# Optimization experiments

Hardware: AMD Instinct MI355X
Metric: run time of the kernel (lower is better)

## Reference

```python
import jax, jax.numpy as jnp
import numpy as np
from jax.scipy.special import logsumexp

D, E, V = 512, 4, 32000
B, L = 1, 1024


def setup_inputs() -> dict:
    key = jax.random.key(0)
    ks = jax.random.split(key, 5)
    s = 0.02
    return {
        "hidden_states": jax.random.normal(ks[0], (B, L, D), dtype=jnp.float32),
        "W_prior": jax.random.normal(ks[1], (D, E), dtype=jnp.float32) * s,
        "b_prior": jnp.zeros((E,), dtype=jnp.float32),
        "W_latent": jax.random.normal(ks[2], (D, E * D), dtype=jnp.float32) * s,
        "b_latent": jnp.zeros((E * D,), dtype=jnp.float32),
        "W_dec": jax.random.normal(ks[3], (D, V), dtype=jnp.float32) * s,
        "b_dec": jnp.zeros((V,), dtype=jnp.float32),
    }


def reference(hidden_states, W_prior, b_prior, W_latent, b_latent, W_dec, b_dec):
    # hidden_states: [B, L, D]
    b, l, d = hidden_states.shape
    e = W_prior.shape[1]
    # mixture coefficients (split_hidden=False path): softmax over experts
    mix_logits = hidden_states @ W_prior + b_prior                 # [B, L, E]
    log_coef = jax.nn.log_softmax(mix_logits, axis=-1)             # [B, L, E]
    # per-expert latent projections with tanh
    latent = jnp.tanh(hidden_states @ W_latent + b_latent)         # [B, L, E*D]
    latent = latent.reshape(b, l, e, d)                            # [B, L, E, D]
    # shared decoder to vocab
    logits = jnp.einsum("bled,dv->blev", latent, W_dec) + b_dec    # [B, L, E, V]
    logp = jax.nn.log_softmax(logits, axis=-1)                     # [B, L, E, V]
    # log(sum_e coef_e * softmax_e) == logsumexp_e(log_coef_e + log_softmax_e)
    out = logsumexp(logp + log_coef[..., None], axis=2)            # [B, L, V]
    return out
```

## Files before the change

kernel.cpp:

```cpp
#include <hip/hip_runtime.h>
#include <hip/hip_bf16.h>
#include <hip/hip_fp16.h>
#include <math.h>


#define D_ 512
#define E_ 4
#define V_ 32000
#define L_ 1024
#define AROWS (L_ * E_)

#define SA_ 0x7D7D7D7D
#define SB_ 0x7B7B7B7B

typedef __attribute__((ext_vector_type(8))) short s16x8;
typedef __attribute__((ext_vector_type(4))) float f32x4;
typedef __attribute__((ext_vector_type(2))) float f32x2;
typedef __attribute__((ext_vector_type(4))) int i32x4;
typedef __attribute__((ext_vector_type(8))) int i32x8;
typedef __attribute__((ext_vector_type(4))) unsigned int u32x4;
typedef const __attribute__((address_space(1))) char* gp1_t;
typedef __attribute__((address_space(3))) char* lp3_t;

__device__ __forceinline__ void gload_lds16(const void* g, void* l) {
  __builtin_amdgcn_global_load_lds((gp1_t)g, (lp3_t)l, 16, 0, 0);
}

#define PREP_DEC  8000
#define PREP_LAT  (PREP_DEC + 1024)
#define PREP_CVT  (PREP_LAT + 512)
#define PREP_PRI  (PREP_CVT + 256)
#define PREP_TOT  (PREP_PRI + 16)

__global__ __launch_bounds__(256) void prep_kernel(
    const float* __restrict__ hs, const float* __restrict__ W_prior,
    const float* __restrict__ b_prior, const float* __restrict__ W_latent,
    const float* __restrict__ W_dec,
    __hip_bfloat16* __restrict__ hs_bf, __hip_bfloat16* __restrict__ WlatT,
    unsigned char* __restrict__ WdecT8, float* __restrict__ log_coef,
    float* __restrict__ S) {
  __shared__ float tileS[64 * 33];
  const int b = blockIdx.x;
  const int tid = threadIdx.x;

  if (b < PREP_DEC) {
    const int vb = (b % 1000) * 32;
    const int db = (b / 1000) * 64;
    {
      const int r = tid >> 2, c0 = (tid & 3) * 8;
      const float* src = W_dec + (size_t)(db + r) * V_ + vb + c0;
      float4 a0 = *(const float4*)src;
      float4 a1 = *(const float4*)(src + 4);
      float* t = &tileS[r * 33 + c0];
      t[0] = a0.x; t[1] = a0.y; t[2] = a0.z; t[3] = a0.w;
      t[4] = a1.x; t[5] = a1.y; t[6] = a1.z; t[7] = a1.w;
    }
    __syncthreads();
    {
      const int vr = tid >> 3, d0 = (tid & 7) * 8;
      float t8[8];
      #pragma unroll
      for (int j = 0; j < 8; ++j) t8[j] = tileS[(d0 + j) * 33 + vr] * 16.f;
      unsigned int u0 = 0, u1 = 0;
      u0 = __builtin_amdgcn_cvt_pk_fp8_f32(t8[0], t8[1], u0, false);
      u0 = __builtin_amdgcn_cvt_pk_fp8_f32(t8[2], t8[3], u0, true);
      u1 = __builtin_amdgcn_cvt_pk_fp8_f32(t8[4], t8[5], u1, false);
      u1 = __builtin_amdgcn_cvt_pk_fp8_f32(t8[6], t8[7], u1, true);
      uint2 uu = {u0, u1};
      *(uint2*)&WdecT8[(size_t)(vb + vr) * D_ + db + d0] = uu;
    }
  } else if (b < PREP_LAT) {
    const int bb = b - PREP_DEC;
    const int cb = (bb & 63) * 32, rb = (bb >> 6) * 32;
    const int C = E_ * D_, R = D_;
    const int tx = tid & 31, ty = tid >> 5;
    #pragma unroll
    for (int j = 0; j < 32; j += 8)
      tileS[(ty + j) * 33 + tx] = W_latent[(size_t)(rb + ty + j) * C + cb + tx];
    __syncthreads();
    #pragma unroll
    for (int j = 0; j < 32; j += 8)
      WlatT[(size_t)(cb + ty + j) * R + rb + tx] = __float2bfloat16(tileS[tx * 33 + ty + j]);
  } else if (b < PREP_CVT) {
    int i = ((b - PREP_LAT) * 256 + tid) * 4;
    float4 v = *(const float4*)(hs + i);
    hs_bf[i + 0] = __float2bfloat16(v.x);
    hs_bf[i + 1] = __float2bfloat16(v.y);
    hs_bf[i + 2] = __float2bfloat16(v.z);
    hs_bf[i + 3] = __float2bfloat16(v.w);
  } else if (b < PREP_PRI) {
    int t = (b - PREP_CVT) * 4 + (tid >> 6);
    int lane = tid & 63;
    float a0 = 0.f, a1 = 0.f, a2 = 0.f, a3 = 0.f;
    for (int d = lane; d < D_; d += 64) {
      float h = hs[t * D_ + d];
      float4 w = ((const float4*)W_prior)[d];
      a0 += h * w.x; a1 += h * w.y; a2 += h * w.z; a3 += h * w.w;
    }
    #pragma unroll
    for (int off = 32; off > 0; off >>= 1) {
      a0 += __shfl_xor(a0, off);
      a1 += __shfl_xor(a1, off);
      a2 += __shfl_xor(a2, off);
      a3 += __shfl_xor(a3, off);
    }
    a0 += b_prior[0]; a1 += b_prior[1]; a2 += b_prior[2]; a3 += b_prior[3];
    float mx = fmaxf(fmaxf(a0, a1), fmaxf(a2, a3));
    float ls = mx + logf(expf(a0 - mx) + expf(a1 - mx) + expf(a2 - mx) + expf(a3 - mx));
    if (lane == 0) {
      log_coef[t * 4 + 0] = a0 - ls;
      log_coef[t * 4 + 1] = a1 - ls;
      log_coef[t * 4 + 2] = a2 - ls;
      log_coef[t * 4 + 3] = a3 - ls;
    }
  } else {
    S[(b - PREP_PRI) * 256 + tid] = 0.f;
  }
}

__global__ void qk_kernel(const float* __restrict__ log_coef, const float* __restrict__ S,
                          float* __restrict__ q) {
  int i = blockIdx.x * blockDim.x + threadIdx.x;
  if (i < AROWS) q[i] = __expf(log_coef[i]) / S[i];
}

__global__ __launch_bounds__(256, 2) void latent_gemm(
    const __hip_bfloat16* __restrict__ Abf, const __hip_bfloat16* __restrict__ BT,
    const float* __restrict__ b_latent, unsigned char* __restrict__ latent8) {
  __shared__ short As[128 * 32];
  __shared__ short Bs[128 * 32];
  const int tid = threadIdx.x;
  const int wave = tid >> 6, lane = tid & 63;
  const int wm = wave >> 1, wn = wave & 1;
  const int m0 = blockIdx.y * 128;
  const int n0 = blockIdx.x * 128;
  const int lrow = lane & 15;
  const int kgrp = lane >> 4;
  const int srow = wave * 16 + (lane >> 2);
  const int scol = (lane & 3) * 8;

  f32x4 acc[4][4];
  #pragma unroll
  for (int mt = 0; mt < 4; ++mt)
    #pragma unroll
    for (int nt = 0; nt < 4; ++nt) acc[mt][nt] = f32x4{0.f, 0.f, 0.f, 0.f};

  for (int kt = 0; kt < 16; ++kt) {
    const int k0 = kt * 32;
    #pragma unroll
    for (int j = 0; j < 2; ++j) {
      const int row = j * 64 + srow;
      gload_lds16(Abf + (size_t)(m0 + row) * D_ + k0 + scol, &As[(j * 256 + wave * 64) * 8]);
      gload_lds16(BT + (size_t)(n0 + row) * D_ + k0 + scol, &Bs[(j * 256 + wave * 64) * 8]);
    }
    __syncthreads();
    s16x8 af[4], bfr[4];
    #pragma unroll
    for (int mt = 0; mt < 4; ++mt) af[mt] = *(const s16x8*)&As[(wm * 64 + mt * 16 + lrow) * 32 + kgrp * 8];
    #pragma unroll
    for (int nt = 0; nt < 4; ++nt) bfr[nt] = *(const s16x8*)&Bs[(wn * 64 + nt * 16 + lrow) * 32 + kgrp * 8];
    #pragma unroll
    for (int mt = 0; mt < 4; ++mt)
      #pragma unroll
      for (int nt = 0; nt < 4; ++nt)
        acc[mt][nt] = __builtin_amdgcn_mfma_f32_16x16x32_bf16(af[mt], bfr[nt], acc[mt][nt], 0, 0, 0);
    __syncthreads();
  }

  float blat[4];
  #pragma unroll
  for (int nt = 0; nt < 4; ++nt) blat[nt] = b_latent[n0 + wn * 64 + nt * 16 + lrow];
  #pragma unroll
  for (int mt = 0; mt < 4; ++mt)
    #pragma unroll
    for (int r = 0; r < 4; ++r) {
      const int row = m0 + wm * 64 + mt * 16 + kgrp * 4 + r;
      #pragma unroll
      for (int nt = 0; nt < 4; ++nt) {
        const int col = n0 + wn * 64 + nt * 16 + lrow;
        float v = tanhf(acc[mt][nt][r] + blat[nt]) * 4.f;
        int u = __builtin_amdgcn_cvt_pk_fp8_f32(v, v, 0, false);
        latent8[(size_t)row * (E_ * D_) + col] = (unsigned char)(u & 0xff);
      }
    }
}

template <int MODE>
__global__ __launch_bounds__(256, 2) void mos_gemm(
    const unsigned char* __restrict__ A8,
    const unsigned char* __restrict__ W8,
    const float* __restrict__ b_dec,
    const float* __restrict__ q,
    float* __restrict__ S,
    float* __restrict__ out,
    unsigned int* __restrict__ pbuf) {
  const int bid = blockIdx.x;
  const int xcd = bid & 7;
  const int idx = bid >> 3;
  const int mg = xcd >> 2;
  const int vg = xcd & 3;
  const int vt = vg * 63 + (idx >> 4);
  const int mtile = mg * 16 + (idx & 15);
  if (vt >= V_ / 128) return;
  const int m0 = mtile * 128;
  const int v0 = vt * 128;

  __shared__ __attribute__((aligned(16))) unsigned char As[128 * 128];
  __shared__ __attribute__((aligned(16))) unsigned char Bs[128 * 128];
  const int tid = threadIdx.x;
  const int wave = tid >> 6, lane = tid & 63;
  const int wm = wave >> 1, wn = wave & 1;
  const int lrow = lane & 15;
  const int kgrp = lane >> 4;
  const int srow8 = wave * 8 + (lane >> 3);
  const int schunk = lane & 7;

  float bdec[4];
  #pragma unroll
  for (int nt = 0; nt < 4; ++nt) bdec[nt] = b_dec[v0 + wn * 64 + nt * 16 + lrow];

  f32x4 acc[4][4];
  #pragma unroll
  for (int mt = 0; mt < 4; ++mt)
    #pragma unroll
    for (int nt = 0; nt < 4; ++nt) acc[mt][nt] = f32x4{0.f, 0.f, 0.f, 0.f};

  for (int kt = 0; kt < 4; ++kt) {
    const int kb = kt * 128;
    #pragma unroll
    for (int j = 0; j < 4; ++j) {
      const int row = j * 32 + srow8;
      const int sc = (schunk ^ (row & 7)) * 16;
      gload_lds16(A8 + (size_t)(m0 + row) * D_ + kb + sc, &As[(j * 32 + wave * 8) * 128]);
      gload_lds16(W8 + (size_t)(v0 + row) * D_ + kb + sc, &Bs[(j * 32 + wave * 8) * 128]);
    }
    __syncthreads();
    i32x8 af[4], bfr[4];
    #pragma unroll
    for (int mt = 0; mt < 4; ++mt) {
      const int row = wm * 64 + mt * 16 + lrow;
      const int s = lrow & 7;
      i32x4 lo = *(const i32x4*)&As[row * 128 + (((kgrp * 2) ^ s) * 16)];
      i32x4 hi = *(const i32x4*)&As[row * 128 + (((kgrp * 2 + 1) ^ s) * 16)];
      af[mt] = __builtin_shufflevector(lo, hi, 0, 1, 2, 3, 4, 5, 6, 7);
    }
    #pragma unroll
    for (int nt = 0; nt < 4; ++nt) {
      const int row = wn * 64 + nt * 16 + lrow;
      const int s = lrow & 7;
      i32x4 lo = *(const i32x4*)&Bs[row * 128 + (((kgrp * 2) ^ s) * 16)];
      i32x4 hi = *(const i32x4*)&Bs[row * 128 + (((kgrp * 2 + 1) ^ s) * 16)];
      bfr[nt] = __builtin_shufflevector(lo, hi, 0, 1, 2, 3, 4, 5, 6, 7);
    }
    #pragma unroll
    for (int mt = 0; mt < 4; ++mt)
      #pragma unroll
      for (int nt = 0; nt < 4; ++nt)
        acc[mt][nt] = __builtin_amdgcn_mfma_scale_f32_16x16x128_f8f6f4(
            af[mt], bfr[nt], acc[mt][nt], 0, 0, 0, SA_, 0, SB_);
    __syncthreads();
  }

  if constexpr (MODE == 1 || MODE == 3) {
    #pragma unroll
    for (int mt = 0; mt < 4; ++mt) {
      const int row4 = m0 + wm * 64 + mt * 16 + kgrp * 4;
      const int token = row4 >> 2;
      float p0 = 0.f, p1 = 0.f, p2 = 0.f, p3 = 0.f;
      #pragma unroll
      for (int nt = 0; nt < 4; ++nt) {
        float e0 = __expf(acc[mt][nt][0] + bdec[nt]);
        float e1 = __expf(acc[mt][nt][1] + bdec[nt]);
        float e2 = __expf(acc[mt][nt][2] + bdec[nt]);
        float e3 = __expf(acc[mt][nt][3] + bdec[nt]);
        p0 += e0; p1 += e1; p2 += e2; p3 += e3;
        if constexpr (MODE == 3) {
          const int v = v0 + wn * 64 + nt * 16 + lrow;
          int u = 0;
          u = __builtin_amdgcn_cvt_pk_fp8_f32(e0, e1, u, false);
          u = __builtin_amdgcn_cvt_pk_fp8_f32(e2, e3, u, true);
          __builtin_nontemporal_store((unsigned int)u, &pbuf[(size_t)token * V_ + v]);
        }
      }
      #pragma unroll
      for (int off = 1; off < 16; off <<= 1) {
        p0 += __shfl_xor(p0, off);
        p1 += __shfl_xor(p1, off);
        p2 += __shfl_xor(p2, off);
        p3 += __shfl_xor(p3, off);
      }
      if (lrow == 0) {
        atomicAdd(&S[row4 + 0], p0);
        atomicAdd(&S[row4 + 1], p1);
        atomicAdd(&S[row4 + 2], p2);
        atomicAdd(&S[row4 + 3], p3);
      }
    }
  } else {
    #pragma unroll
    for (int mt = 0; mt < 4; ++mt) {
      const int row4 = m0 + wm * 64 + mt * 16 + kgrp * 4;
      const float4 qv = *(const float4*)&q[row4];
      const int token = row4 >> 2;
      #pragma unroll
      for (int nt = 0; nt < 4; ++nt) {
        float v = qv.x * __expf(acc[mt][nt][0] + bdec[nt]) +
                  qv.y * __expf(acc[mt][nt][1] + bdec[nt]) +
                  qv.z * __expf(acc[mt][nt][2] + bdec[nt]) +
                  qv.w * __expf(acc[mt][nt][3] + bdec[nt]);
        out[(size_t)token * V_ + v0 + wn * 64 + nt * 16 + lrow] = __logf(v);
      }
    }
  }
}

__global__ __launch_bounds__(256) void combine_kernel(
    const unsigned int* __restrict__ pbuf,
    const float* __restrict__ lc, const float* __restrict__ S,
    float* __restrict__ out) {
  const int t = blockIdx.y;
  const int v = blockIdx.x * 1024 + threadIdx.x * 4;
  if (v >= V_) return;
  const float4 lcv = ((const float4*)lc)[t];
  const float4 Sv = ((const float4*)S)[t];
  const float q0 = __expf(lcv.x) / Sv.x;
  const float q1 = __expf(lcv.y) / Sv.y;
  const float q2 = __expf(lcv.z) / Sv.z;
  const float q3 = __expf(lcv.w) / Sv.w;
  u32x4 u = __builtin_nontemporal_load((const u32x4*)(pbuf + (size_t)t * V_ + v));
  float4 o;
  #pragma unroll
  for (int j = 0; j < 4; ++j) {
    unsigned int w = u[j];
    f32x2 lo = __builtin_amdgcn_cvt_pk_f32_fp8(w, false);
    f32x2 hi = __builtin_amdgcn_cvt_pk_f32_fp8(w, true);
    float s = q0 * lo.x + q1 * lo.y + q2 * hi.x + q3 * hi.y;
    ((float*)&o)[j] = __logf(s);
  }
  *(float4*)&out[(size_t)t * V_ + v] = o;
}

extern "C" void kernel_launch(void* const* d_in, const int* in_sizes, int n_in,
                              void* d_out, int out_size, void* d_ws, size_t ws_size,
                              hipStream_t stream) {
  const float* hs       = (const float*)d_in[0];
  const float* W_prior  = (const float*)d_in[1];
  const float* b_prior  = (const float*)d_in[2];
  const float* W_latent = (const float*)d_in[3];
  const float* b_latent = (const float*)d_in[4];
  const float* W_dec    = (const float*)d_in[5];
  const float* b_dec    = (const float*)d_in[6];
  float* out = (float*)d_out;

  char* ws = (char*)d_ws;
  __hip_bfloat16* hs_bf   = (__hip_bfloat16*)(ws);
  __hip_bfloat16* WlatT   = (__hip_bfloat16*)(ws + (1u << 20));
  unsigned char*  latent8 = (unsigned char*)(ws + 3u * (1u << 20));
  unsigned char*  WdecT8  = (unsigned char*)(ws + 5u * (1u << 20));
  float* log_coef = (float*)(ws + 22u * (1u << 20));
  float* S = log_coef + AROWS;
  float* q = S + AROWS;
  unsigned int* pbuf = (unsigned int*)(ws + 23u * (1u << 20));

  const size_t needA = 23u * (1u << 20) + (size_t)L_ * V_ * 4;
  const bool pathA = ws_size >= needA;

  prep_kernel<<<PREP_TOT, 256, 0, stream>>>(hs, W_prior, b_prior, W_latent, W_dec,
                                            hs_bf, WlatT, WdecT8, log_coef, S);
  latent_gemm<<<dim3((E_ * D_) / 128, L_ / 128), 256, 0, stream>>>(hs_bf, WlatT, b_latent, latent8);

  if (pathA) {
    mos_gemm<3><<<8 * 16 * 63, 256, 0, stream>>>(latent8, WdecT8, b_dec, nullptr, S, nullptr, pbuf);
    combine_kernel<<<dim3(32, L_), 256, 0, stream>>>(pbuf, log_coef, S, out);
  } else {
    mos_gemm<1><<<8 * 16 * 63, 256, 0, stream>>>(latent8, WdecT8, b_dec, nullptr, S, nullptr, nullptr);
    qk_kernel<<<(AROWS + 255) / 256, 256, 0, stream>>>(log_coef, S, q);
    mos_gemm<2><<<8 * 16 * 63, 256, 0, stream>>>(latent8, WdecT8, b_dec, q, nullptr, out, nullptr);
  }
}
```

Before: 357.9 us.

## Use fragment-native LDS layout, DPP row reductions, and MFMA priority in decoder GEMM

Each lane now loads its own MFMA fragment directly from global memory into LDS, so fragments are read back with contiguous lane-indexed accesses and no XOR swizzle or per-row address math. The k-loop is fully unrolled, and s_setprio raises wave priority around the MFMA block. The 16-lane shuffle-xor reduction of the partial exp sums becomes a DPP row_shr prefix sum, with lane 15 doing the atomics. This targets LDS bank conflicts, address arithmetic and reduction overhead. The cost is uncoalesced global reads, since each lane now fetches 16 bytes from a different row.

```diff
diff --git a/kernel.cpp b/kernel.cpp
--- a/kernel.cpp
+++ b/kernel.cpp
@@ -24,6 +24,19 @@
 
 __device__ __forceinline__ void gload_lds16(const void* g, void* l) {
   __builtin_amdgcn_global_load_lds((gp1_t)g, (lp3_t)l, 16, 0, 0);
+}
+
+__device__ __forceinline__ float dpp_row16_sum(float x) {
+  int t;
+  t = __builtin_amdgcn_update_dpp(0, __float_as_int(x), 0x111, 0xF, 0xF, true);
+  x += __int_as_float(t);
+  t = __builtin_amdgcn_update_dpp(0, __float_as_int(x), 0x112, 0xF, 0xF, true);
+  x += __int_as_float(t);
+  t = __builtin_amdgcn_update_dpp(0, __float_as_int(x), 0x114, 0xF, 0xF, true);
+  x += __int_as_float(t);
+  t = __builtin_amdgcn_update_dpp(0, __float_as_int(x), 0x118, 0xF, 0xF, true);
+  x += __int_as_float(t);
+  return x;
 }
 
 #define PREP_DEC  8000
@@ -205,15 +218,25 @@
   const int m0 = mtile * 128;
   const int v0 = vt * 128;
 
-  __shared__ __attribute__((aligned(16))) unsigned char As[128 * 128];
-  __shared__ __attribute__((aligned(16))) unsigned char Bs[128 * 128];
+  __shared__ __attribute__((aligned(16))) unsigned char As[16384];
+  __shared__ __attribute__((aligned(16))) unsigned char Bs[16384];
+
   const int tid = threadIdx.x;
   const int wave = tid >> 6, lane = tid & 63;
   const int wm = wave >> 1, wn = wave & 1;
   const int lrow = lane & 15;
   const int kgrp = lane >> 4;
-  const int srow8 = wave * 8 + (lane >> 3);
-  const int schunk = lane & 7;
+
+  const unsigned char* gA[4];
+  const unsigned char* gB[4];
+  #pragma unroll
+  for (int c = 0; c < 4; ++c) {
+    const int r = c * 4 + wave;
+    const int row = (r >> 1) * 16 + lrow;
+    const int kof = kgrp * 32 + (r & 1) * 16;
+    gA[c] = A8 + (size_t)(m0 + row) * D_ + kof;
+    gB[c] = W8 + (size_t)(v0 + row) * D_ + kof;
+  }
 
   float bdec[4];
   #pragma unroll
@@ -225,39 +248,36 @@
     #pragma unroll
     for (int nt = 0; nt < 4; ++nt) acc[mt][nt] = f32x4{0.f, 0.f, 0.f, 0.f};
 
+  #pragma unroll
   for (int kt = 0; kt < 4; ++kt) {
     const int kb = kt * 128;
     #pragma unroll
-    for (int j = 0; j < 4; ++j) {
-      const int row = j * 32 + srow8;
-      const int sc = (schunk ^ (row & 7)) * 16;
-      gload_lds16(A8 + (size_t)(m0 + row) * D_ + kb + sc, &As[(j * 32 + wave * 8) * 128]);
-      gload_lds16(W8 + (size_t)(v0 + row) * D_ + kb + sc, &Bs[(j * 32 + wave * 8) * 128]);
-    }
-    __syncthreads();
-    i32x8 af[4], bfr[4];
+    for (int c = 0; c < 4; ++c) {
+      gload_lds16(gA[c] + kb, &As[(c * 4 + wave) * 1024]);
+      gload_lds16(gB[c] + kb, &Bs[(c * 4 + wave) * 1024]);
+    }
+    __syncthreads();
+    i32x8 bf8[4];
+    #pragma unroll
+    for (int nt = 0; nt < 4; ++nt) {
+      const int g = wn * 4 + nt;
+      i32x4 lo = *(const i32x4*)&Bs[g * 2048 + lane * 16];
+      i32x4 hi = *(const i32x4*)&Bs[g * 2048 + 1024 + lane * 16];
+      bf8[nt] = __builtin_shufflevector(lo, hi, 0, 1, 2, 3, 4, 5, 6, 7);
+    }
+    __builtin_amdgcn_s_setprio(1);
     #pragma unroll
     for (int mt = 0; mt < 4; ++mt) {
-      const int row = wm * 64 + mt * 16 + lrow;
-      const int s = lrow & 7;
-      i32x4 lo = *(const i32x4*)&As[row * 128 + (((kgrp * 2) ^ s) * 16)];
-      i32x4 hi = *(const i32x4*)&As[row * 128 + (((kgrp * 2 + 1) ^ s) * 16)];
-      af[mt] = __builtin_shufflevector(lo, hi, 0, 1, 2, 3, 4, 5, 6, 7);
-    }
-    #pragma unroll
-    for (int nt = 0; nt < 4; ++nt) {
-      const int row = wn * 64 + nt * 16 + lrow;
-      const int s = lrow & 7;
-      i32x4 lo = *(const i32x4*)&Bs[row * 128 + (((kgrp * 2) ^ s) * 16)];
-      i32x4 hi = *(const i32x4*)&Bs[row * 128 + (((kgrp * 2 + 1) ^ s) * 16)];
-      bfr[nt] = __builtin_shufflevector(lo, hi, 0, 1, 2, 3, 4, 5, 6, 7);
-    }
-    #pragma unroll
-    for (int mt = 0; mt < 4; ++mt)
+      const int g = wm * 4 + mt;
+      i32x4 lo = *(const i32x4*)&As[g * 2048 + lane * 16];
+      i32x4 hi = *(const i32x4*)&As[g * 2048 + 1024 + lane * 16];
+      i32x8 a = __builtin_shufflevector(lo, hi, 0, 1, 2, 3, 4, 5, 6, 7);
       #pragma unroll
       for (int nt = 0; nt < 4; ++nt)
         acc[mt][nt] = __builtin_amdgcn_mfma_scale_f32_16x16x128_f8f6f4(
-            af[mt], bfr[nt], acc[mt][nt], 0, 0, 0, SA_, 0, SB_);
+            a, bf8[nt], acc[mt][nt], 0, 0, 0, SA_, 0, SB_);
+    }
+    __builtin_amdgcn_s_setprio(0);
     __syncthreads();
   }
 
@@ -282,14 +302,11 @@
           __builtin_nontemporal_store((unsigned int)u, &pbuf[(size_t)token * V_ + v]);
         }
       }
-      #pragma unroll
-      for (int off = 1; off < 16; off <<= 1) {
-        p0 += __shfl_xor(p0, off);
-        p1 += __shfl_xor(p1, off);
-        p2 += __shfl_xor(p2, off);
-        p3 += __shfl_xor(p3, off);
-      }
-      if (lrow == 0) {
+      p0 = dpp_row16_sum(p0);
+      p1 = dpp_row16_sum(p1);
+      p2 = dpp_row16_sum(p2);
+      p3 = dpp_row16_sum(p3);
+      if (lrow == 15) {
         atomicAdd(&S[row4 + 0], p0);
         atomicAdd(&S[row4 + 1], p1);
         atomicAdd(&S[row4 + 2], p2);
```

Result: slower. 403.2 us (+12.6%).

## Stage fp8 probability tiles in LDS for coalesced stores; DPP reductions; fewer combine blocks

Applied to the files above, without the earlier changes.

The MODE 3 epilogue now writes packed fp8 exp values into a swizzled LDS buffer (reusing As), then after a barrier emits 16-byte coalesced nontemporal stores to pbuf. Before, each lane issued a scattered 4-byte store. Row-16 reductions switch from shfl_xor to DPP row_shr adds, with lane 15 doing the atomics. The combine kernel uses 8 blocks per token, each looping over 4000 vocab entries instead of 32 single-shot blocks, which cuts block count but lowers parallelism per token. The change adds a block-wide sync and LDS traffic in the GEMM epilogue.

```diff
diff --git a/kernel.cpp b/kernel.cpp
--- a/kernel.cpp
+++ b/kernel.cpp
@@ -24,6 +24,19 @@
 
 __device__ __forceinline__ void gload_lds16(const void* g, void* l) {
   __builtin_amdgcn_global_load_lds((gp1_t)g, (lp3_t)l, 16, 0, 0);
+}
+
+__device__ __forceinline__ float dpp_row16_sum(float x) {
+  int t;
+  t = __builtin_amdgcn_update_dpp(0, __float_as_int(x), 0x111, 0xF, 0xF, true);
+  x += __int_as_float(t);
+  t = __builtin_amdgcn_update_dpp(0, __float_as_int(x), 0x112, 0xF, 0xF, true);
+  x += __int_as_float(t);
+  t = __builtin_amdgcn_update_dpp(0, __float_as_int(x), 0x114, 0xF, 0xF, true);
+  x += __int_as_float(t);
+  t = __builtin_amdgcn_update_dpp(0, __float_as_int(x), 0x118, 0xF, 0xF, true);
+  x += __int_as_float(t);
+  return x;
 }
 
 #define PREP_DEC  8000
@@ -262,10 +275,11 @@
   }
 
   if constexpr (MODE == 1 || MODE == 3) {
+    unsigned int* pls = (unsigned int*)As;
     #pragma unroll
     for (int mt = 0; mt < 4; ++mt) {
       const int row4 = m0 + wm * 64 + mt * 16 + kgrp * 4;
-      const int token = row4 >> 2;
+      const int tloc = wm * 16 + mt * 4 + kgrp;
       float p0 = 0.f, p1 = 0.f, p2 = 0.f, p3 = 0.f;
       #pragma unroll
       for (int nt = 0; nt < 4; ++nt) {
@@ -275,25 +289,35 @@
         float e3 = __expf(acc[mt][nt][3] + bdec[nt]);
         p0 += e0; p1 += e1; p2 += e2; p3 += e3;
         if constexpr (MODE == 3) {
-          const int v = v0 + wn * 64 + nt * 16 + lrow;
+          const int vloc = wn * 64 + nt * 16 + lrow;
           int u = 0;
           u = __builtin_amdgcn_cvt_pk_fp8_f32(e0, e1, u, false);
           u = __builtin_amdgcn_cvt_pk_fp8_f32(e2, e3, u, true);
-          __builtin_nontemporal_store((unsigned int)u, &pbuf[(size_t)token * V_ + v]);
+          pls[tloc * 128 + ((vloc + 8 * tloc) & 127)] = (unsigned int)u;
         }
       }
-      #pragma unroll
-      for (int off = 1; off < 16; off <<= 1) {
-        p0 += __shfl_xor(p0, off);
-        p1 += __shfl_xor(p1, off);
-        p2 += __shfl_xor(p2, off);
-        p3 += __shfl_xor(p3, off);
-      }
-      if (lrow == 0) {
+      p0 = dpp_row16_sum(p0);
+      p1 = dpp_row16_sum(p1);
+      p2 = dpp_row16_sum(p2);
+      p3 = dpp_row16_sum(p3);
+      if (lrow == 15) {
         atomicAdd(&S[row4 + 0], p0);
         atomicAdd(&S[row4 + 1], p1);
         atomicAdd(&S[row4 + 2], p2);
         atomicAdd(&S[row4 + 3], p3);
+      }
+    }
+    if constexpr (MODE == 3) {
+      __syncthreads();
+      const int tokg = m0 >> 2;
+      #pragma unroll
+      for (int j = 0; j < 4; ++j) {
+        const int slot = j * 256 + tid;
+        const int tl = slot >> 5;
+        const int vswz = (slot & 31) * 4;
+        const int vloc = (vswz - 8 * tl) & 127;
+        u32x4 u = *(const u32x4*)&pls[tl * 128 + vswz];
+        __builtin_nontemporal_store(u, (u32x4*)&pbuf[(size_t)(tokg + tl) * V_ + v0 + vloc]);
       }
     }
   } else {
@@ -319,25 +343,29 @@
     const float* __restrict__ lc, const float* __restrict__ S,
     float* __restrict__ out) {
   const int t = blockIdx.y;
-  const int v = blockIdx.x * 1024 + threadIdx.x * 4;
-  if (v >= V_) return;
+  const int vbase = blockIdx.x * (V_ / 8);
+  const int vend = vbase + (V_ / 8);
   const float4 lcv = ((const float4*)lc)[t];
   const float4 Sv = ((const float4*)S)[t];
   const float q0 = __expf(lcv.x) / Sv.x;
   const float q1 = __expf(lcv.y) / Sv.y;
   const float q2 = __expf(lcv.z) / Sv.z;
   const float q3 = __expf(lcv.w) / Sv.w;
-  u32x4 u = __builtin_nontemporal_load((const u32x4*)(pbuf + (size_t)t * V_ + v));
-  float4 o;
-  #pragma unroll
-  for (int j = 0; j < 4; ++j) {
-    unsigned int w = u[j];
-    f32x2 lo = __builtin_amdgcn_cvt_pk_f32_fp8(w, false);
-    f32x2 hi = __builtin_amdgcn_cvt_pk_f32_fp8(w, true);
-    float s = q0 * lo.x + q1 * lo.y + q2 * hi.x + q3 * hi.y;
-    ((float*)&o)[j] = __logf(s);
-  }
-  *(float4*)&out[(size_t)t * V_ + v] = o;
+  const unsigned int* prow = pbuf + (size_t)t * V_;
+  float* orow = out + (size_t)t * V_;
+  for (int v = vbase + threadIdx.x * 4; v < vend; v += 1024) {
+    u32x4 u = __builtin_nontemporal_load((const u32x4*)(prow + v));
+    float4 o;
+    #pragma unroll
+    for (int j = 0; j < 4; ++j) {
+      unsigned int w = u[j];
+      f32x2 lo = __builtin_amdgcn_cvt_pk_f32_fp8(w, false);
+      f32x2 hi = __builtin_amdgcn_cvt_pk_f32_fp8(w, true);
+      float s = q0 * lo.x + q1 * lo.y + q2 * hi.x + q3 * hi.y;
+      ((float*)&o)[j] = __logf(s);
+    }
+    *(float4*)(orow + v) = o;
+  }
 }
 
 extern "C" void kernel_launch(void* const* d_in, const int* in_sizes, int n_in,
@@ -371,7 +399,7 @@
 
   if (pathA) {
     mos_gemm<3><<<8 * 16 * 63, 256, 0, stream>>>(latent8, WdecT8, b_dec, nullptr, S, nullptr, pbuf);
-    combine_kernel<<<dim3(32, L_), 256, 0, stream>>>(pbuf, log_coef, S, out);
+    combine_kernel<<<dim3(8, L_), 256, 0, stream>>>(pbuf, log_coef, S, out);
   } else {
     mos_gemm<1><<<8 * 16 * 63, 256, 0, stream>>>(latent8, WdecT8, b_dec, nullptr, S, nullptr, nullptr);
     qk_kernel<<<(AROWS + 255) / 256, 256, 0, stream>>>(log_coef, S, q);
```

Result: no change. 358.1 us (+0.1%).
